# Kernel optimization log

Hardware: AMD Instinct MI355X
Metric: run time of the kernel (lower is better)

The kernel has to match this reference:

```python
import jax, jax.numpy as jnp
import numpy as np

D_K = 64  # matches init_kwargs d_k


def setup_inputs() -> dict:
    key = jax.random.key(0)
    k0, k1, k2, k3 = jax.random.split(key, 4)
    B, H, TW, L, D = 4, 8, 20, 256, 64
    q = jax.random.normal(k0, (B, H, TW, D), dtype=jnp.float32)
    k = jax.random.normal(k1, (B, H, L, D), dtype=jnp.float32)
    v = jax.random.normal(k2, (B, H, L, D), dtype=jnp.float32)
    bias = jax.random.normal(k3, (B, L, H, TW, L), dtype=jnp.float32)
    return {"q": q, "k": k, "v": v, "bias": bias}


def reference(q, k, v, bias):
    # q: [B,H,TW,D]; k,v: [B,H,L,D]; bias: [B,L,H,TW,L]
    B, H, TW, D = q.shape
    L = k.shape[2]
    # The torch code expands q over the L axis before matmul with k^T; since
    # QK^T does not depend on that axis, compute it once and broadcast.
    scores = jnp.einsum('bhwd,bhld->bhwl', q, k) / jnp.sqrt(jnp.asarray(D_K, q.dtype))
    # weight: [B,L,H,TW,L]; dropout-before-softmax is identity in eval mode
    w = jax.nn.softmax(scores[:, None, :, :, :] + bias, axis=-1)
    # transpose(1,2).view(B,H,L*TW,L) @ v, then transpose(1,2).view(B,L*TW,H*D)
    attn = jnp.einsum('blhwk,bhkd->blwhd', w, v)  # [B,L,TW,H,D]
    return attn.reshape(B, L * TW, H * D)
```

## Files before the change

### kernel.cpp

```cpp
#include <hip/hip_runtime.h>
#include <hip/hip_bf16.h>

#define NB 4
#define NH 8
#define NW 20
#define NL 256
#define ND 64
#define ROWGRPS 40

typedef __attribute__((ext_vector_type(8))) short bf16x8;
typedef __attribute__((ext_vector_type(4))) short short4v;
typedef __attribute__((ext_vector_type(4))) float f32x4;

static __device__ __forceinline__ short f2bf(float f) {
  __hip_bfloat16 h = __float2bfloat16(f);
  short s;
  __builtin_memcpy(&s, &h, 2);
  return s;
}
static __device__ __forceinline__ float bf2f(short s) {
  __hip_bfloat16 h;
  __builtin_memcpy(&h, &s, 2);
  return __bfloat162float(h);
}

__global__ __launch_bounds__(256) void qk_scores_kernel(
    const float* __restrict__ q, const float* __restrict__ k,
    float* __restrict__ scores) {
  const int bid = blockIdx.x;
  const int w = bid % NW;
  const int bh = bid / NW;
  const int l = threadIdx.x;
  const float4* qrow = (const float4*)(q + ((long)bh * NW + w) * ND);
  const float4* krow = (const float4*)(k + ((long)bh * NL + l) * ND);
  float acc = 0.f;
#pragma unroll
  for (int j = 0; j < ND / 4; ++j) {
    float4 a = qrow[j];
    float4 c = krow[j];
    acc += a.x * c.x + a.y * c.y + a.z * c.z + a.w * c.w;
  }
  scores[((long)bh * NW + w) * NL + l] = acc * 0.125f;
}

__global__ __launch_bounds__(512, 4) void attn_kernel(
    const float* __restrict__ v, const float* __restrict__ bias,
    const float* __restrict__ scores, float* __restrict__ out) {
  __shared__ short sv_hi[NL * ND];
  __shared__ short sv_lo[NL * ND];

  const int t = threadIdx.x;
  const int bid = blockIdx.x;
  const int rg = bid % ROWGRPS;
  const int h = (bid / ROWGRPS) % NH;
  const int b = bid / (ROWGRPS * NH);

  {
    const int d = t & 63;
    const int kb = (t >> 6) * 4;
    const float* vp = v + ((long)(b * NH + h)) * NL * ND + d;
#pragma unroll
    for (int i = 0; i < 8; ++i) {
      const int k0 = kb + i * 32;
      float f0 = vp[(long)(k0 + 0) * ND];
      float f1 = vp[(long)(k0 + 1) * ND];
      float f2 = vp[(long)(k0 + 2) * ND];
      float f3 = vp[(long)(k0 + 3) * ND];
      short4v hi, lo;
      hi.x = f2bf(f0); lo.x = f2bf(f0 - bf2f(hi.x));
      hi.y = f2bf(f1); lo.y = f2bf(f1 - bf2f(hi.y));
      hi.z = f2bf(f2); lo.z = f2bf(f2 - bf2f(hi.z));
      hi.w = f2bf(f3); lo.w = f2bf(f3 - bf2f(hi.w));
      const int off = (d << 9) + ((k0 << 1) ^ ((d & 7) << 4));
      *(short4v*)((char*)sv_hi + off) = hi;
      *(short4v*)((char*)sv_lo + off) = lo;
    }
  }
  __syncthreads();

  const int wave = t >> 6;
  const int lane = t & 63;
  const int rl = lane & 15;
  const int g = lane >> 4;
  const int r0 = rg * 128 + wave * 16;
  const int row = r0 + rl;
  const int li = row / NW;
  const int wi = row % NW;

  const float* brow = bias + (((long)(b * NL + li) * NH + h) * NW + wi) * NL;
  const float* srow = scores + ((long)((b * NH + h) * NW + wi)) * NL;

  f32x4 acc[4];
#pragma unroll
  for (int dt = 0; dt < 4; ++dt) acc[dt] = (f32x4){0.f, 0.f, 0.f, 0.f};
  float den = 0.f;

  const char* hb = (const char*)sv_hi;
  const char* lb = (const char*)sv_lo;

#pragma unroll 2
  for (int s = 0; s < 8; ++s) {
    const int k0 = s * 32 + g * 8;
    float4 b0 = *(const float4*)(brow + k0);
    float4 b1 = *(const float4*)(brow + k0 + 4);
    float4 s0 = *(const float4*)(srow + k0);
    float4 s1 = *(const float4*)(srow + k0 + 4);
    float p[8];
    p[0] = __expf(b0.x + s0.x);
    p[1] = __expf(b0.y + s0.y);
    p[2] = __expf(b0.z + s0.z);
    p[3] = __expf(b0.w + s0.w);
    p[4] = __expf(b1.x + s1.x);
    p[5] = __expf(b1.y + s1.y);
    p[6] = __expf(b1.z + s1.z);
    p[7] = __expf(b1.w + s1.w);
    den += ((p[0] + p[1]) + (p[2] + p[3])) + ((p[4] + p[5]) + (p[6] + p[7]));
    bf16x8 phi, plo;
#pragma unroll
    for (int j = 0; j < 8; ++j) {
      short hj = f2bf(p[j]);
      phi[j] = hj;
      plo[j] = f2bf(p[j] - bf2f(hj));
    }
#pragma unroll
    for (int dt = 0; dt < 4; ++dt) {
      const int d = dt * 16 + rl;
      const int off = (d << 9) + ((k0 << 1) ^ ((d & 7) << 4));
      bf16x8 vh = *(const bf16x8*)(hb + off);
      bf16x8 vl = *(const bf16x8*)(lb + off);
      acc[dt] = __builtin_amdgcn_mfma_f32_16x16x32_bf16(phi, vh, acc[dt], 0, 0, 0);
      acc[dt] = __builtin_amdgcn_mfma_f32_16x16x32_bf16(phi, vl, acc[dt], 0, 0, 0);
      acc[dt] = __builtin_amdgcn_mfma_f32_16x16x32_bf16(plo, vh, acc[dt], 0, 0, 0);
    }
  }

  float dsum = den + __shfl_xor(den, 16);
  dsum += __shfl_xor(dsum, 32);

  float* ob = out + ((long)b * (NL * NW)) * (NH * ND) + h * ND + rl;
#pragma unroll
  for (int i = 0; i < 4; ++i) {
    const int crow = (lane >> 4) * 4 + i;
    const float rinv = 1.0f / __shfl(dsum, crow);
    float* op = ob + (long)(r0 + crow) * (NH * ND);
    op[0]  = acc[0][i] * rinv;
    op[16] = acc[1][i] * rinv;
    op[32] = acc[2][i] * rinv;
    op[48] = acc[3][i] * rinv;
  }
}

extern "C" void kernel_launch(void* const* d_in, const int* in_sizes, int n_in,
                              void* d_out, int out_size, void* d_ws, size_t ws_size,
                              hipStream_t stream) {
  (void)in_sizes; (void)n_in; (void)out_size; (void)ws_size;
  const float* q = (const float*)d_in[0];
  const float* k = (const float*)d_in[1];
  const float* v = (const float*)d_in[2];
  const float* bias = (const float*)d_in[3];
  float* out = (float*)d_out;
  float* scores = (float*)d_ws;

  qk_scores_kernel<<<NB * NH * NW, NL, 0, stream>>>(q, k, scores);
  attn_kernel<<<NB * NH * ROWGRPS, 512, 0, stream>>>(v, bias, scores, out);
}
```

Measured before the change: 265.9 us.

## Stage V in two halves, prefetch bias one step ahead, use nontemporal IO

The V tile is now staged into LDS in two 128-row halves, which halves shared memory per block and raises the occupancy hint from 4 to 5 blocks. Bias and score loads are software-pipelined one iteration ahead of the MFMA body, and the first bias load is issued before V staging. Bias reads and output writes use nontemporal hints to avoid polluting the cache. The trade-off is extra block barriers between the halves and a second staging pass in the middle of compute.

```diff
diff --git a/kernel.cpp b/kernel.cpp
--- a/kernel.cpp
+++ b/kernel.cpp
@@ -31,52 +31,29 @@
   const int w = bid % NW;
   const int bh = bid / NW;
   const int l = threadIdx.x;
-  const float4* qrow = (const float4*)(q + ((long)bh * NW + w) * ND);
-  const float4* krow = (const float4*)(k + ((long)bh * NL + l) * ND);
+  const f32x4* qrow = (const f32x4*)(q + ((long)bh * NW + w) * ND);
+  const f32x4* krow = (const f32x4*)(k + ((long)bh * NL + l) * ND);
   float acc = 0.f;
 #pragma unroll
   for (int j = 0; j < ND / 4; ++j) {
-    float4 a = qrow[j];
-    float4 c = krow[j];
+    f32x4 a = qrow[j];
+    f32x4 c = krow[j];
     acc += a.x * c.x + a.y * c.y + a.z * c.z + a.w * c.w;
   }
   scores[((long)bh * NW + w) * NL + l] = acc * 0.125f;
 }
 
-__global__ __launch_bounds__(512, 4) void attn_kernel(
+__global__ __launch_bounds__(512, 5) void attn_kernel(
     const float* __restrict__ v, const float* __restrict__ bias,
     const float* __restrict__ scores, float* __restrict__ out) {
-  __shared__ short sv_hi[NL * ND];
-  __shared__ short sv_lo[NL * ND];
+  __shared__ short sv_hi[128 * ND];
+  __shared__ short sv_lo[128 * ND];
 
   const int t = threadIdx.x;
   const int bid = blockIdx.x;
   const int rg = bid % ROWGRPS;
   const int h = (bid / ROWGRPS) % NH;
   const int b = bid / (ROWGRPS * NH);
-
-  {
-    const int d = t & 63;
-    const int kb = (t >> 6) * 4;
-    const float* vp = v + ((long)(b * NH + h)) * NL * ND + d;
-#pragma unroll
-    for (int i = 0; i < 8; ++i) {
-      const int k0 = kb + i * 32;
-      float f0 = vp[(long)(k0 + 0) * ND];
-      float f1 = vp[(long)(k0 + 1) * ND];
-      float f2 = vp[(long)(k0 + 2) * ND];
-      float f3 = vp[(long)(k0 + 3) * ND];
-      short4v hi, lo;
-      hi.x = f2bf(f0); lo.x = f2bf(f0 - bf2f(hi.x));
-      hi.y = f2bf(f1); lo.y = f2bf(f1 - bf2f(hi.y));
-      hi.z = f2bf(f2); lo.z = f2bf(f2 - bf2f(hi.z));
-      hi.w = f2bf(f3); lo.w = f2bf(f3 - bf2f(hi.w));
-      const int off = (d << 9) + ((k0 << 1) ^ ((d & 7) << 4));
-      *(short4v*)((char*)sv_hi + off) = hi;
-      *(short4v*)((char*)sv_lo + off) = lo;
-    }
-  }
-  __syncthreads();
 
   const int wave = t >> 6;
   const int lane = t & 63;
@@ -90,6 +67,39 @@
   const float* brow = bias + (((long)(b * NL + li) * NH + h) * NW + wi) * NL;
   const float* srow = scores + ((long)((b * NH + h) * NW + wi)) * NL;
 
+  const int sd = t & 63;
+  const int kb4 = (t >> 6) * 4;
+  const float* vbase = v + ((long)(b * NH + h)) * NL * ND + sd;
+  auto stage = [&](int kh) {
+    const float* vp = vbase + (long)(kh * 128) * ND;
+#pragma unroll
+    for (int i = 0; i < 4; ++i) {
+      const int kl = kb4 + i * 32;
+      float f0 = vp[(long)(kl + 0) * ND];
+      float f1 = vp[(long)(kl + 1) * ND];
+      float f2 = vp[(long)(kl + 2) * ND];
+      float f3 = vp[(long)(kl + 3) * ND];
+      short4v hi, lo;
+      hi.x = f2bf(f0); lo.x = f2bf(f0 - bf2f(hi.x));
+      hi.y = f2bf(f1); lo.y = f2bf(f1 - bf2f(hi.y));
+      hi.z = f2bf(f2); lo.z = f2bf(f2 - bf2f(hi.z));
+      hi.w = f2bf(f3); lo.w = f2bf(f3 - bf2f(hi.w));
+      const int off = (sd << 8) + ((kl << 1) ^ ((sd & 7) << 4));
+      *(short4v*)((char*)sv_hi + off) = hi;
+      *(short4v*)((char*)sv_lo + off) = lo;
+    }
+  };
+
+  f32x4 nb0, nb1, ns0, ns1;
+  auto issue = [&](int s) {
+    const float* bp = brow + s * 32 + g * 8;
+    const float* sp = srow + s * 32 + g * 8;
+    nb0 = __builtin_nontemporal_load((const f32x4*)bp);
+    nb1 = __builtin_nontemporal_load((const f32x4*)(bp + 4));
+    ns0 = *(const f32x4*)sp;
+    ns1 = *(const f32x4*)(sp + 4);
+  };
+
   f32x4 acc[4];
 #pragma unroll
   for (int dt = 0; dt < 4; ++dt) acc[dt] = (f32x4){0.f, 0.f, 0.f, 0.f};
@@ -98,13 +108,7 @@
   const char* hb = (const char*)sv_hi;
   const char* lb = (const char*)sv_lo;
 
-#pragma unroll 2
-  for (int s = 0; s < 8; ++s) {
-    const int k0 = s * 32 + g * 8;
-    float4 b0 = *(const float4*)(brow + k0);
-    float4 b1 = *(const float4*)(brow + k0 + 4);
-    float4 s0 = *(const float4*)(srow + k0);
-    float4 s1 = *(const float4*)(srow + k0 + 4);
+  auto body = [&](int sl, f32x4 b0, f32x4 b1, f32x4 s0, f32x4 s1) {
     float p[8];
     p[0] = __expf(b0.x + s0.x);
     p[1] = __expf(b0.y + s0.y);
@@ -122,16 +126,36 @@
       phi[j] = hj;
       plo[j] = f2bf(p[j] - bf2f(hj));
     }
+    const int k0l = sl * 32 + g * 8;
 #pragma unroll
     for (int dt = 0; dt < 4; ++dt) {
       const int d = dt * 16 + rl;
-      const int off = (d << 9) + ((k0 << 1) ^ ((d & 7) << 4));
+      const int off = (d << 8) + ((k0l << 1) ^ ((d & 7) << 4));
       bf16x8 vh = *(const bf16x8*)(hb + off);
       bf16x8 vl = *(const bf16x8*)(lb + off);
       acc[dt] = __builtin_amdgcn_mfma_f32_16x16x32_bf16(phi, vh, acc[dt], 0, 0, 0);
       acc[dt] = __builtin_amdgcn_mfma_f32_16x16x32_bf16(phi, vl, acc[dt], 0, 0, 0);
       acc[dt] = __builtin_amdgcn_mfma_f32_16x16x32_bf16(plo, vh, acc[dt], 0, 0, 0);
     }
+  };
+
+  issue(0);
+  stage(0);
+  __syncthreads();
+#pragma unroll
+  for (int s = 0; s < 4; ++s) {
+    f32x4 b0 = nb0, b1 = nb1, s0 = ns0, s1 = ns1;
+    issue(s + 1);
+    body(s, b0, b1, s0, s1);
+  }
+  __syncthreads();
+  stage(1);
+  __syncthreads();
+#pragma unroll
+  for (int s = 4; s < 8; ++s) {
+    f32x4 b0 = nb0, b1 = nb1, s0 = ns0, s1 = ns1;
+    if (s < 7) issue(s + 1);
+    body(s - 4, b0, b1, s0, s1);
   }
 
   float dsum = den + __shfl_xor(den, 16);
@@ -143,10 +167,10 @@
     const int crow = (lane >> 4) * 4 + i;
     const float rinv = 1.0f / __shfl(dsum, crow);
     float* op = ob + (long)(r0 + crow) * (NH * ND);
-    op[0]  = acc[0][i] * rinv;
-    op[16] = acc[1][i] * rinv;
-    op[32] = acc[2][i] * rinv;
-    op[48] = acc[3][i] * rinv;
+    __builtin_nontemporal_store(acc[0][i] * rinv, op);
+    __builtin_nontemporal_store(acc[1][i] * rinv, op + 16);
+    __builtin_nontemporal_store(acc[2][i] * rinv, op + 32);
+    __builtin_nontemporal_store(acc[3][i] * rinv, op + 48);
   }
 }
 
```

Result: slower. 301.2 us (+13.3%).
